# Kernel optimization log

Measured on AMD Instinct MI355X. Metric: run time of the kernel, lower is better.

Reference implementation:

```python
import jax, jax.numpy as jnp
import numpy as np

B = 64        # graphs in batch
N = 512       # nodes per graph (equal-size graphs)
DEG = 16      # avg degree
D_IN = 512
D_OUT = 512
RATIO = 0.5
K = int(np.ceil(RATIO * N))  # nodes kept per graph by SAGPool
NUM_NODES = B * N


def setup_inputs() -> dict:
    key = jax.random.key(0)
    ks = jax.random.split(key, 12)
    e_per = N * DEG
    offs = (jnp.arange(B, dtype=jnp.int32) * N)[:, None]
    src = (jax.random.randint(ks[0], (B, e_per), 0, N, dtype=jnp.int32) + offs).reshape(-1)
    dst = (jax.random.randint(ks[1], (B, e_per), 0, N, dtype=jnp.int32) + offs).reshape(-1)
    x = jax.random.normal(ks[2], (NUM_NODES, D_IN), jnp.float32)
    sc = 0.05  # small init so relu/tanh stay in sane range
    return {
        'x': x,
        'src': src,
        'dst': dst,
        'W1': jax.random.normal(ks[3], (D_IN, D_OUT), jnp.float32) * sc,
        'b1': jnp.zeros((D_OUT,), jnp.float32),
        'W2': jax.random.normal(ks[4], (D_OUT, D_OUT), jnp.float32) * sc,
        'b2': jnp.zeros((D_OUT,), jnp.float32),
        'sW1': jax.random.normal(ks[5], (D_OUT, 1), jnp.float32) * sc,
        'sb1': jnp.zeros((1,), jnp.float32),
        'sW2': jax.random.normal(ks[6], (D_OUT, 1), jnp.float32) * sc,
        'sb2': jnp.zeros((1,), jnp.float32),
    }


def graph_conv(src, dst, x, W, b, n_nodes):
    """DGL GraphConv, norm='both': D_in^{-1/2} A D_out^{-1/2} x W + b.
    W applied before aggregation (mathematically identical, cheaper when out_dim small)."""
    ones = jnp.ones(src.shape[0], x.dtype)
    deg_out = jax.ops.segment_sum(ones, src, num_segments=n_nodes)
    deg_in = jax.ops.segment_sum(ones, dst, num_segments=n_nodes)
    norm_out = jnp.maximum(deg_out, 1.0) ** -0.5  # DGL clamps deg to min 1
    norm_in = jnp.maximum(deg_in, 1.0) ** -0.5
    h = (x @ W) * norm_out[:, None]               # [n, out]
    m = jax.ops.segment_sum(h[src], dst, num_segments=n_nodes)  # gather+scatter over edges
    return m * norm_in[:, None] + b


def reference(x, src, dst, W1, b1, W2, b2, sW1, sb1, sW2, sb2):
    n = NUM_NODES
    h = jax.nn.relu(graph_conv(src, dst, x, W1, b1, n))   # conv1 + relu, reshape(-1,512) is a no-op
    h = jax.nn.relu(graph_conv(src, dst, h, W2, b2, n))   # conv2 + relu
    # SAGPool: two GraphConv score layers, averaged
    s1 = graph_conv(src, dst, h, sW1, sb1, n)[:, 0]
    s2 = graph_conv(src, dst, h, sW2, sb2, n)[:, 0]
    score = 0.5 * (s1 + s2)                                # [B*N]
    _, top_idx = jax.lax.top_k(score.reshape(B, N), K)     # per-graph top-k, [B, K]
    perm = (top_idx + (jnp.arange(B, dtype=top_idx.dtype) * N)[:, None]).reshape(-1)  # global ids
    pooled = h[perm] * jnp.tanh(score[perm])[:, None]      # [B*K, D_OUT] gated gather
    pb = pooled.reshape(B, K, D_OUT)
    # readout: max || sum per graph
    g_out = jnp.concatenate([pb.max(axis=1), pb.sum(axis=1)], axis=-1)  # [B, 2*D_OUT]
    return pooled, g_out
```

## Files before the change

kernel.cpp:

```cpp
#include <hip/hip_runtime.h>
#include <math.h>

typedef unsigned short u16;
typedef __attribute__((ext_vector_type(8))) short bf16x8;
typedef __attribute__((ext_vector_type(4))) float f32x4;

#define NN 32768
#define EDGES 524288
#define NB 64
#define NPG 512
#define EPG 8192
#define KEEP 256
#define D 512

__device__ __forceinline__ float b2f(u16 h){ return __uint_as_float(((unsigned)h)<<16); }
__device__ __forceinline__ u16 f2b(float f){
  unsigned u = __float_as_uint(f);
  unsigned r = u + 0x7FFFu + ((u>>16)&1u);
  return (u16)(r>>16);
}

__device__ __forceinline__ void gload16(const void* g, void* l){
  __builtin_amdgcn_global_load_lds((const __attribute__((address_space(1))) void*)g,
                                   (__attribute__((address_space(3))) void*)l, 16, 0, 0);
}

__global__ __launch_bounds__(256) void detect_kernel(const u16* __restrict__ xb, int* __restrict__ flags){
  __shared__ int cnt;
  if (threadIdx.x==0) cnt = 0;
  __syncthreads();
  u16 v = xb[threadIdx.x];
  int e = (v>>7)&0xFF;
  if (e > 140) atomicAdd(&cnt, 1);
  __syncthreads();
  if (threadIdx.x==0){ flags[0] = (cnt > 8) ? 1 : 0; flags[1] = 1; }
}

__global__ __launch_bounds__(512) void graphprep_kernel(
    const int* __restrict__ src, const int* __restrict__ dst,
    float* __restrict__ no, float* __restrict__ ni,
    int* __restrict__ rowp, int* __restrict__ csr)
{
  __shared__ int dego[NPG], degi[NPG], s[NPG], start[NPG], cur[NPG];
  int g = blockIdx.x, n = threadIdx.x;
  dego[n] = 0; degi[n] = 0; cur[n] = 0;
  __syncthreads();
  int ebase = g*EPG;
  #pragma unroll
  for (int i = 0; i < 16; i++){
    int e = ebase + n + i*512;
    atomicAdd(&dego[src[e] & (NPG-1)], 1);
    atomicAdd(&degi[dst[e] & (NPG-1)], 1);
  }
  __syncthreads();
  int di = degi[n];
  s[n] = di;
  __syncthreads();
  for (int off=1; off<NPG; off<<=1){
    int val = (n>=off) ? s[n-off] : 0;
    __syncthreads();
    s[n] += val;
    __syncthreads();
  }
  int excl = s[n] - di;
  start[n] = excl;
  int a = dego[n]; if (a<1) a=1;
  int b = di;      if (b<1) b=1;
  int v = g*NPG + n;
  no[v] = (float)(1.0/sqrt((double)a));
  ni[v] = (float)(1.0/sqrt((double)b));
  rowp[v] = ebase + excl;
  if (g == NB-1 && n == NPG-1) rowp[NN] = EDGES;
  __syncthreads();
  #pragma unroll
  for (int i = 0; i < 16; i++){
    int e = ebase + n + i*512;
    int dl = dst[e] & (NPG-1);
    int pos = atomicAdd(&cur[dl], 1);
    csr[ebase + start[dl] + pos] = src[e];
  }
}

__global__ __launch_bounds__(512) void bcvt_kernel(const int* __restrict__ flags,
    const void* b1, const void* b2, const void* sW1, const void* sW2,
    const void* sb1, const void* sb2,
    float* b1c, float* b2c, float* sW1c, float* sW2c, float* sbc)
{
  int t = threadIdx.x;
  int f = flags[0];
  #define CV(p,i) (f ? ((const float*)(p))[i] : b2f(((const u16*)(p))[i]))
  b1c[t]  = CV(b1, t);
  b2c[t]  = CV(b2, t);
  sW1c[t] = CV(sW1, t);
  sW2c[t] = CV(sW2, t);
  if (t==0){ sbc[0] = CV(sb1,0); sbc[1] = CV(sb2,0); }
  #undef CV
}

__global__ void tsplit_kernel(const int* __restrict__ flags, const void* __restrict__ W,
                              u16* __restrict__ WTh, u16* __restrict__ WTl){
  __shared__ float tile[32][33];
  int f = flags[0];
  int bx = blockIdx.x*32, by = blockIdx.y*32;
  int tx = threadIdx.x, ty = threadIdx.y;
  #pragma unroll
  for (int i=0;i<4;i++){
    size_t idx = (size_t)(by+ty+i*8)*D + bx+tx;
    tile[ty+i*8][tx] = f ? ((const float*)W)[idx] : b2f(((const u16*)W)[idx]);
  }
  __syncthreads();
  #pragma unroll
  for (int i=0;i<4;i++){
    float v = tile[tx][ty+i*8];
    u16 h = f2b(v);
    size_t o = (size_t)(bx+ty+i*8)*D + by+tx;
    WTh[o] = h;
    WTl[o] = f2b(v - b2f(h));
  }
}

__global__ __launch_bounds__(256) void xsplit_kernel(const void* __restrict__ X,
    const int* __restrict__ flags, u16* __restrict__ Xh, u16* __restrict__ Xl)
{
  size_t i = ((size_t)blockIdx.x*256 + threadIdx.x)*4;
  float v0,v1,v2,v3;
  if (flags[0]){
    float4 f = *(const float4*)((const float*)X + i);
    v0=f.x; v1=f.y; v2=f.z; v3=f.w;
  } else {
    ushort4 uv = *(const ushort4*)((const u16*)X + i);
    v0=b2f(uv.x); v1=b2f(uv.y); v2=b2f(uv.z); v3=b2f(uv.w);
  }
  ushort4 hh, hl;
  hh.x=f2b(v0); hl.x=f2b(v0-b2f(hh.x));
  hh.y=f2b(v1); hl.y=f2b(v1-b2f(hh.y));
  hh.z=f2b(v2); hl.z=f2b(v2-b2f(hh.z));
  hh.w=f2b(v3); hl.w=f2b(v3-b2f(hh.w));
  *(ushort4*)(Xh+i) = hh;
  *(ushort4*)(Xl+i) = hl;
}


__device__ __forceinline__ void gemm_tile256(int id, int& brow, int& bcol){
  int xcd = id & 7, k = id >> 3;
  brow = (xcd + 8*(k >> 1)) * 256;
  bcol = (k & 1) * 256;
}

__global__ __launch_bounds__(512, 2) void gemm256(
    const u16* __restrict__ Ahg, const u16* __restrict__ Alg,
    const u16* __restrict__ BTh, const u16* __restrict__ BTl,
    float* __restrict__ C, const float* __restrict__ rowscale)
{
  __shared__ alignas(16) u16 lds[2][4][8192];
  int t = threadIdx.x;
  int brow, bcol;
  gemm_tile256(blockIdx.x, brow, bcol);
  int wid = t>>6, lane = t&63;
  int wr = wid>>2, wc = wid&3;
  int q = lane>>4, r = lane&15;
  f32x4 acc[8][4] = {};

  int c0 = wid*128 + lane, c1 = c0 + 64;
  int q0 = c0>>8, r0 = c0&255, q1 = c1>>8, r1 = c1&255;
  const u16* sA0h = Ahg + (size_t)(brow+r0)*D + q0*8;
  const u16* sA1h = Ahg + (size_t)(brow+r1)*D + q1*8;
  const u16* sA0l = Alg + (size_t)(brow+r0)*D + q0*8;
  const u16* sA1l = Alg + (size_t)(brow+r1)*D + q1*8;
  const u16* sB0h = BTh + (size_t)(bcol+r0)*D + q0*8;
  const u16* sB1h = BTh + (size_t)(bcol+r1)*D + q1*8;
  const u16* sB0l = BTl + (size_t)(bcol+r0)*D + q0*8;
  const u16* sB1l = BTl + (size_t)(bcol+r1)*D + q1*8;

  #define STAGEK(B, KT) { int ko = (KT)*32; \
    gload16(sA0h+ko, &lds[B][0][c0*8]); gload16(sA1h+ko, &lds[B][0][c1*8]); \
    gload16(sA0l+ko, &lds[B][1][c0*8]); gload16(sA1l+ko, &lds[B][1][c1*8]); \
    gload16(sB0h+ko, &lds[B][2][c0*8]); gload16(sB1h+ko, &lds[B][2][c1*8]); \
    gload16(sB0l+ko, &lds[B][3][c0*8]); gload16(sB1l+ko, &lds[B][3][c1*8]); }

  STAGEK(0, 0)
  asm volatile("s_waitcnt vmcnt(0)" ::: "memory");
  __syncthreads();
  int cur = 0;
  for (int kt=0; kt<16; kt++){
    if (kt < 15) STAGEK(cur^1, kt+1)
    bf16x8 fbh[4], fbl[4];
    #pragma unroll
    for (int n=0;n<4;n++){
      fbh[n] = *(const bf16x8*)(&lds[cur][2][(q*256 + wc*64 + n*16 + r)*8]);
      fbl[n] = *(const bf16x8*)(&lds[cur][3][(q*256 + wc*64 + n*16 + r)*8]);
    }
    __builtin_amdgcn_s_setprio(1);
    #pragma unroll
    for (int m=0;m<8;m++){
      bf16x8 fah = *(const bf16x8*)(&lds[cur][0][(q*256 + wr*128 + m*16 + r)*8]);
      bf16x8 fal = *(const bf16x8*)(&lds[cur][1][(q*256 + wr*128 + m*16 + r)*8]);
      #pragma unroll
      for (int n=0;n<4;n++){
        acc[m][n] = __builtin_amdgcn_mfma_f32_16x16x32_bf16(fah, fbh[n], acc[m][n], 0,0,0);
        acc[m][n] = __builtin_amdgcn_mfma_f32_16x16x32_bf16(fah, fbl[n], acc[m][n], 0,0,0);
        acc[m][n] = __builtin_amdgcn_mfma_f32_16x16x32_bf16(fal, fbh[n], acc[m][n], 0,0,0);
      }
    }
    __builtin_amdgcn_s_setprio(0);
    asm volatile("s_waitcnt vmcnt(0)" ::: "memory");
    __syncthreads();
    cur ^= 1;
  }
  #undef STAGEK

  #pragma unroll
  for (int m=0;m<8;m++){
    int rowb = brow + wr*128 + m*16 + q*4;
    #pragma unroll
    for (int n=0;n<4;n++){
      int col = bcol + wc*64 + n*16 + r;
      #pragma unroll
      for (int g=0; g<4; g++){
        int row = rowb + g;
        C[(size_t)row*D + col] = acc[m][n][g] * rowscale[row];
      }
    }
  }
}


__global__ __launch_bounds__(256) void agg_kernel(
    const float* __restrict__ Y, const int* __restrict__ rowp,
    const int* __restrict__ csr, const float* __restrict__ ni,
    const float* __restrict__ bias, float* __restrict__ H,
    u16* __restrict__ Hh, u16* __restrict__ Hl,
    const float* __restrict__ sW1, const float* __restrict__ sW2,
    float* __restrict__ t1, float* __restrict__ t2, int mode)
{
  int i = blockIdx.x;
  int xcd = i & 7, j = i >> 3;
  int half = threadIdx.x >> 7;
  int t = threadIdx.x & 127;
  int lane = threadIdx.x & 63;
  int v = (xcd + 8*(j >> 8))*NPG + ((j & 255)*2 + half);
  int rp0 = rowp[v], rp1 = rowp[v+1];
  const float4* Yv = (const float4*)Y;
  float4 a = {0.f,0.f,0.f,0.f};
  for (int eb = rp0; eb < rp1; eb += 64){
    int cnt = rp1 - eb; if (cnt > 64) cnt = 64;
    int idx = (lane < cnt) ? csr[eb + lane] : 0;
    int e = 0;
    for (; e+8 <= cnt; e += 8){
      int u0 = __shfl(idx, e),   u1 = __shfl(idx, e+1);
      int u2 = __shfl(idx, e+2), u3 = __shfl(idx, e+3);
      int u4 = __shfl(idx, e+4), u5 = __shfl(idx, e+5);
      int u6 = __shfl(idx, e+6), u7 = __shfl(idx, e+7);
      float4 y0 = Yv[(size_t)u0*128 + t];
      float4 y1 = Yv[(size_t)u1*128 + t];
      float4 y2 = Yv[(size_t)u2*128 + t];
      float4 y3 = Yv[(size_t)u3*128 + t];
      float4 y4 = Yv[(size_t)u4*128 + t];
      float4 y5 = Yv[(size_t)u5*128 + t];
      float4 y6 = Yv[(size_t)u6*128 + t];
      float4 y7 = Yv[(size_t)u7*128 + t];
      a.x += ((y0.x + y1.x) + (y2.x + y3.x)) + ((y4.x + y5.x) + (y6.x + y7.x));
      a.y += ((y0.y + y1.y) + (y2.y + y3.y)) + ((y4.y + y5.y) + (y6.y + y7.y));
      a.z += ((y0.z + y1.z) + (y2.z + y3.z)) + ((y4.z + y5.z) + (y6.z + y7.z));
      a.w += ((y0.w + y1.w) + (y2.w + y3.w)) + ((y4.w + y5.w) + (y6.w + y7.w));
    }
    for (; e+4 <= cnt; e += 4){
      int u0 = __shfl(idx, e),   u1 = __shfl(idx, e+1);
      int u2 = __shfl(idx, e+2), u3 = __shfl(idx, e+3);
      float4 y0 = Yv[(size_t)u0*128 + t];
      float4 y1 = Yv[(size_t)u1*128 + t];
      float4 y2 = Yv[(size_t)u2*128 + t];
      float4 y3 = Yv[(size_t)u3*128 + t];
      a.x += (y0.x + y1.x) + (y2.x + y3.x);
      a.y += (y0.y + y1.y) + (y2.y + y3.y);
      a.z += (y0.z + y1.z) + (y2.z + y3.z);
      a.w += (y0.w + y1.w) + (y2.w + y3.w);
    }
    for (; e < cnt; e++){
      int u = __shfl(idx, e);
      float4 y = Yv[(size_t)u*128 + t];
      a.x += y.x; a.y += y.y; a.z += y.z; a.w += y.w;
    }
  }
  float w = ni[v];
  float4 b4 = ((const float4*)bias)[t];
  float4 rr;
  rr.x = fmaxf(a.x*w + b4.x, 0.f);
  rr.y = fmaxf(a.y*w + b4.y, 0.f);
  rr.z = fmaxf(a.z*w + b4.z, 0.f);
  rr.w = fmaxf(a.w*w + b4.w, 0.f);

  if (mode == 0){
    ushort4 hh, hl;
    hh.x = f2b(rr.x); hl.x = f2b(rr.x - b2f(hh.x));
    hh.y = f2b(rr.y); hl.y = f2b(rr.y - b2f(hh.y));
    hh.z = f2b(rr.z); hl.z = f2b(rr.z - b2f(hh.z));
    hh.w = f2b(rr.w); hl.w = f2b(rr.w - b2f(hh.w));
    *(ushort4*)(Hh + (size_t)v*D + t*4) = hh;
    *(ushort4*)(Hl + (size_t)v*D + t*4) = hl;
  } else {
    ((float4*)H)[(size_t)v*128 + t] = rr;
    float4 w1 = ((const float4*)sW1)[t];
    float4 w2 = ((const float4*)sW2)[t];
    float p1 = rr.x*w1.x + rr.y*w1.y + rr.z*w1.z + rr.w*w1.w;
    float p2 = rr.x*w2.x + rr.y*w2.y + rr.z*w2.z + rr.w*w2.w;
    #pragma unroll
    for (int off=32; off>=1; off>>=1){
      p1 += __shfl_xor(p1, off);
      p2 += __shfl_xor(p2, off);
    }
    __shared__ float red1[4], red2[4];
    int wv = threadIdx.x>>6;
    if (lane==0){ red1[wv] = p1; red2[wv] = p2; }
    __syncthreads();
    if (t==0){
      t1[v] = red1[half*2] + red1[half*2+1];
      t2[v] = red2[half*2] + red2[half*2+1];
    }
  }
}


__global__ __launch_bounds__(512) void scoretopk_kernel(
    const float* __restrict__ t1, const float* __restrict__ t2,
    const int* __restrict__ rowp, const int* __restrict__ csr,
    const float* __restrict__ no, const float* __restrict__ ni,
    const float* __restrict__ sbc,
    int* __restrict__ perm, float* __restrict__ gate)
{
  __shared__ unsigned long long key[NPG];
  __shared__ float scl[NPG];
  int g = blockIdx.x, n = threadIdx.x;
  int v = g*NPG + n;
  double a1 = 0.0, a2 = 0.0;
  int rp1 = rowp[v+1];
  for (int e=rowp[v]; e<rp1; e++){
    int u = csr[e];
    double w = (double)no[u];
    a1 += (double)t1[u]*w;
    a2 += (double)t2[u]*w;
  }
  double wi = (double)ni[v];
  double s1 = a1*wi + (double)sbc[0];
  double s2 = a2*wi + (double)sbc[1];
  float s = (float)(0.5*(s1+s2));
  scl[n] = s;
  unsigned u = __float_as_uint(s);
  u = (u & 0x80000000u) ? ~u : (u | 0x80000000u);
  unsigned kd = ~u;
  key[n] = ((unsigned long long)kd<<32) | (unsigned)n;
  __syncthreads();
  for (int k=2; k<=NPG; k<<=1){
    for (int j=k>>1; j>0; j>>=1){
      int ixj = n ^ j;
      if (ixj > n){
        unsigned long long a = key[n], b = key[ixj];
        bool up = ((n & k) == 0);
        if ((a > b) == up){ key[n] = b; key[ixj] = a; }
      }
      __syncthreads();
    }
  }
  if (n < KEEP){
    unsigned long long e = key[n];
    int idx = (int)(e & 0xFFFFFFFFull);
    perm[g*KEEP + n] = g*NPG + idx;
    gate[g*KEEP + n] = tanhf(scl[idx]);
  }
}


__global__ __launch_bounds__(256) void readout_kernel(const float* __restrict__ H,
    const int* __restrict__ perm, const float* __restrict__ gate,
    float* __restrict__ outp, float* __restrict__ outg)
{
  __shared__ int sp[KEEP];
  __shared__ float sg[KEEP];
  __shared__ float4 redmx[128], redsm[128];
  int g = blockIdx.x, t = threadIdx.x;
  int half = t >> 7, c = t & 127;
  sp[t] = perm[g*KEEP + t];
  sg[t] = gate[g*KEEP + t];
  __syncthreads();
  float4 mx = {-INFINITY,-INFINITY,-INFINITY,-INFINITY};
  float4 sm = {0.f,0.f,0.f,0.f};
  for (int rI = half; rI < KEEP; rI += 2){
    int node = sp[rI];
    float gt = sg[rI];
    float4 y = ((const float4*)(H + (size_t)node*D))[c];
    float4 vv;
    vv.x = y.x*gt; vv.y = y.y*gt; vv.z = y.z*gt; vv.w = y.w*gt;
    ((float4*)(outp + (size_t)(g*KEEP + rI)*D))[c] = vv;
    mx.x = fmaxf(mx.x, vv.x); mx.y = fmaxf(mx.y, vv.y);
    mx.z = fmaxf(mx.z, vv.z); mx.w = fmaxf(mx.w, vv.w);
    sm.x += vv.x; sm.y += vv.y; sm.z += vv.z; sm.w += vv.w;
  }
  if (half == 1){ redmx[c] = mx; redsm[c] = sm; }
  __syncthreads();
  if (half == 0){
    float4 omx = redmx[c], osm = redsm[c];
    mx.x = fmaxf(mx.x, omx.x); mx.y = fmaxf(mx.y, omx.y);
    mx.z = fmaxf(mx.z, omx.z); mx.w = fmaxf(mx.w, omx.w);
    sm.x += osm.x; sm.y += osm.y; sm.z += osm.z; sm.w += osm.w;
    ((float4*)(outg + (size_t)g*1024))[c] = mx;
    ((float4*)(outg + (size_t)g*1024 + 512))[c] = sm;
  }
}


extern "C" void kernel_launch(void* const* d_in, const int* in_sizes, int n_in,
                              void* d_out, int out_size, void* d_ws, size_t ws_size,
                              hipStream_t stream)
{
  (void)in_sizes; (void)n_in; (void)out_size; (void)ws_size;
  const void* x   = d_in[0];
  const int* src  = (const int*)d_in[1];
  const int* dst  = (const int*)d_in[2];
  const void* W1  = d_in[3];
  const void* b1  = d_in[4];
  const void* W2  = d_in[5];
  const void* b2  = d_in[6];
  const void* sW1 = d_in[7];
  const void* sb1 = d_in[8];
  const void* sW2 = d_in[9];
  const void* sb2 = d_in[10];
  float* out = (float*)d_out;

  char* ws = (char*)d_ws;
  size_t off = 0;
  auto alloc = [&](size_t bytes){ void* p = ws + off; off += (bytes + 255) & ~(size_t)255; return p; };
  int*   flags  = (int*)  alloc(2*4);
  float* no     = (float*)alloc((size_t)NN*4);
  float* ni     = (float*)alloc((size_t)NN*4);
  int*   rowp   = (int*)  alloc((size_t)(NN+1)*4);
  float* t1     = (float*)alloc((size_t)NN*4);
  float* t2     = (float*)alloc((size_t)NN*4);
  int*   perm   = (int*)  alloc((size_t)NB*KEEP*4);
  float* gate   = (float*)alloc((size_t)NB*KEEP*4);
  float* b1c    = (float*)alloc((size_t)D*4);
  float* b2c    = (float*)alloc((size_t)D*4);
  float* sW1c   = (float*)alloc((size_t)D*4);
  float* sW2c   = (float*)alloc((size_t)D*4);
  float* sbc    = (float*)alloc(2*4);
  u16*   W1Th   = (u16*)  alloc((size_t)D*D*2);
  u16*   W1Tl   = (u16*)  alloc((size_t)D*D*2);
  u16*   W2Th   = (u16*)  alloc((size_t)D*D*2);
  u16*   W2Tl   = (u16*)  alloc((size_t)D*D*2);
  int*   csr    = (int*)  alloc((size_t)EDGES*4);
  u16*   Hh     = (u16*)  alloc((size_t)NN*D*2);
  u16*   Hl     = (u16*)  alloc((size_t)NN*D*2);
  float* Y      = (float*)alloc((size_t)NN*D*4);
  float* H      = (float*)alloc((size_t)NN*D*4);
  u16*   Xh     = (u16*)H;
  u16*   Xl     = Xh + (size_t)NN*D;

  detect_kernel   <<<1, 256, 0, stream>>>((const u16*)x, flags);
  graphprep_kernel<<<NB, 512, 0, stream>>>(src, dst, no, ni, rowp, csr);
  bcvt_kernel     <<<1, 512, 0, stream>>>(flags, b1, b2, sW1, sW2, sb1, sb2,
                                          b1c, b2c, sW1c, sW2c, sbc);
  tsplit_kernel   <<<dim3(16,16), dim3(32,8), 0, stream>>>(flags, W1, W1Th, W1Tl);
  tsplit_kernel   <<<dim3(16,16), dim3(32,8), 0, stream>>>(flags, W2, W2Th, W2Tl);
  xsplit_kernel   <<<(NN*D/4)/256, 256, 0, stream>>>(x, flags, Xh, Xl);

  gemm256<<<256, 512, 0, stream>>>(Xh, Xl, W1Th, W1Tl, Y, no);
  agg_kernel<<<NN/2, 256, 0, stream>>>(Y, rowp, csr, ni, b1c, nullptr, Hh, Hl,
                                       nullptr, nullptr, nullptr, nullptr, 0);
  gemm256<<<256, 512, 0, stream>>>(Hh, Hl, W2Th, W2Tl, Y, no);
  agg_kernel<<<NN/2, 256, 0, stream>>>(Y, rowp, csr, ni, b2c, H, nullptr, nullptr,
                                       sW1c, sW2c, t1, t2, 1);

  scoretopk_kernel<<<NB, 512, 0, stream>>>(t1, t2, rowp, csr, no, ni, sbc, perm, gate);
  readout_kernel  <<<NB, 256, 0, stream>>>(H, perm, gate, out, out + (size_t)NB*KEEP*D);
}
```

Baseline: 345.0 us.

## Fuse small prep kernels, merge score/top-k with readout, store final H in bf16

```diff
diff --git a/kernel.cpp b/kernel.cpp
--- a/kernel.cpp
+++ b/kernel.cpp
@@ -25,15 +25,17 @@
                                    (__attribute__((address_space(3))) void*)l, 16, 0, 0);
 }
 
-__global__ __launch_bounds__(256) void detect_kernel(const u16* __restrict__ xb, int* __restrict__ flags){
-  __shared__ int cnt;
-  if (threadIdx.x==0) cnt = 0;
-  __syncthreads();
-  u16 v = xb[threadIdx.x];
-  int e = (v>>7)&0xFF;
-  if (e > 140) atomicAdd(&cnt, 1);
-  __syncthreads();
-  if (threadIdx.x==0){ flags[0] = (cnt > 8) ? 1 : 0; flags[1] = 1; }
+__device__ __forceinline__ int flag_f32(const u16* __restrict__ xb, int tid){
+  __shared__ int fl;
+  if (tid < 64){
+    u16 v0 = xb[tid*2], v1 = xb[tid*2+1];
+    int c = ((((v0>>7)&0xFF) > 140) ? 1 : 0) + ((((v1>>7)&0xFF) > 140) ? 1 : 0);
+    #pragma unroll
+    for (int o=32; o>=1; o>>=1) c += __shfl_xor(c, o);
+    if (tid == 0) fl = (c > 8) ? 1 : 0;
+  }
+  __syncthreads();
+  return fl;
 }
 
 __global__ __launch_bounds__(512) void graphprep_kernel(
@@ -81,13 +83,13 @@
   }
 }
 
-__global__ __launch_bounds__(512) void bcvt_kernel(const int* __restrict__ flags,
+__global__ __launch_bounds__(512) void bcvt_kernel(const u16* __restrict__ xb,
     const void* b1, const void* b2, const void* sW1, const void* sW2,
     const void* sb1, const void* sb2,
     float* b1c, float* b2c, float* sW1c, float* sW2c, float* sbc)
 {
   int t = threadIdx.x;
-  int f = flags[0];
+  int f = flag_f32(xb, t);
   #define CV(p,i) (f ? ((const float*)(p))[i] : b2f(((const u16*)(p))[i]))
   b1c[t]  = CV(b1, t);
   b2c[t]  = CV(b2, t);
@@ -97,10 +99,16 @@
   #undef CV
 }
 
-__global__ void tsplit_kernel(const int* __restrict__ flags, const void* __restrict__ W,
-                              u16* __restrict__ WTh, u16* __restrict__ WTl){
+__global__ void tsplit_kernel(const u16* __restrict__ xb,
+                              const void* __restrict__ W1, const void* __restrict__ W2,
+                              u16* __restrict__ W1Th, u16* __restrict__ W1Tl,
+                              u16* __restrict__ W2Th, u16* __restrict__ W2Tl){
   __shared__ float tile[32][33];
-  int f = flags[0];
+  int tid = threadIdx.x + threadIdx.y*32;
+  int f = flag_f32(xb, tid);
+  const void* W = blockIdx.z ? W2 : W1;
+  u16* WTh = blockIdx.z ? W2Th : W1Th;
+  u16* WTl = blockIdx.z ? W2Tl : W1Tl;
   int bx = blockIdx.x*32, by = blockIdx.y*32;
   int tx = threadIdx.x, ty = threadIdx.y;
   #pragma unroll
@@ -120,24 +128,27 @@
 }
 
 __global__ __launch_bounds__(256) void xsplit_kernel(const void* __restrict__ X,
-    const int* __restrict__ flags, u16* __restrict__ Xh, u16* __restrict__ Xl)
-{
-  size_t i = ((size_t)blockIdx.x*256 + threadIdx.x)*4;
-  float v0,v1,v2,v3;
-  if (flags[0]){
-    float4 f = *(const float4*)((const float*)X + i);
-    v0=f.x; v1=f.y; v2=f.z; v3=f.w;
-  } else {
-    ushort4 uv = *(const ushort4*)((const u16*)X + i);
-    v0=b2f(uv.x); v1=b2f(uv.y); v2=b2f(uv.z); v3=b2f(uv.w);
-  }
-  ushort4 hh, hl;
-  hh.x=f2b(v0); hl.x=f2b(v0-b2f(hh.x));
-  hh.y=f2b(v1); hl.y=f2b(v1-b2f(hh.y));
-  hh.z=f2b(v2); hl.z=f2b(v2-b2f(hh.z));
-  hh.w=f2b(v3); hl.w=f2b(v3-b2f(hh.w));
-  *(ushort4*)(Xh+i) = hh;
-  *(ushort4*)(Xl+i) = hl;
+    u16* __restrict__ Xh, u16* __restrict__ Xl)
+{
+  int f = flag_f32((const u16*)X, threadIdx.x);
+  size_t stride = (size_t)gridDim.x*256*4;
+  for (size_t i = ((size_t)blockIdx.x*256 + threadIdx.x)*4; i < (size_t)NN*D; i += stride){
+    float v0,v1,v2,v3;
+    if (f){
+      float4 fv = *(const float4*)((const float*)X + i);
+      v0=fv.x; v1=fv.y; v2=fv.z; v3=fv.w;
+    } else {
+      ushort4 uv = *(const ushort4*)((const u16*)X + i);
+      v0=b2f(uv.x); v1=b2f(uv.y); v2=b2f(uv.z); v3=b2f(uv.w);
+    }
+    ushort4 hh, hl;
+    hh.x=f2b(v0); hl.x=f2b(v0-b2f(hh.x));
+    hh.y=f2b(v1); hl.y=f2b(v1-b2f(hh.y));
+    hh.z=f2b(v2); hl.z=f2b(v2-b2f(hh.z));
+    hh.w=f2b(v3); hl.w=f2b(v3-b2f(hh.w));
+    *(ushort4*)(Xh+i) = hh;
+    *(ushort4*)(Xl+i) = hl;
+  }
 }
 
 
@@ -228,7 +239,7 @@
 __global__ __launch_bounds__(256) void agg_kernel(
     const float* __restrict__ Y, const int* __restrict__ rowp,
     const int* __restrict__ csr, const float* __restrict__ ni,
-    const float* __restrict__ bias, float* __restrict__ H,
+    const float* __restrict__ bias,
     u16* __restrict__ Hh, u16* __restrict__ Hl,
     const float* __restrict__ sW1, const float* __restrict__ sW2,
     float* __restrict__ t1, float* __restrict__ t2, int mode)
@@ -299,7 +310,9 @@
     *(ushort4*)(Hh + (size_t)v*D + t*4) = hh;
     *(ushort4*)(Hl + (size_t)v*D + t*4) = hl;
   } else {
-    ((float4*)H)[(size_t)v*128 + t] = rr;
+    ushort4 hb;
+    hb.x = f2b(rr.x); hb.y = f2b(rr.y); hb.z = f2b(rr.z); hb.w = f2b(rr.w);
+    *(ushort4*)(Hh + (size_t)v*D + t*4) = hb;
     float4 w1 = ((const float4*)sW1)[t];
     float4 w2 = ((const float4*)sW2)[t];
     float p1 = rr.x*w1.x + rr.y*w1.y + rr.z*w1.z + rr.w*w1.w;
@@ -321,15 +334,18 @@
 }
 
 
-__global__ __launch_bounds__(512) void scoretopk_kernel(
+__global__ __launch_bounds__(512) void scoretopk_readout_kernel(
     const float* __restrict__ t1, const float* __restrict__ t2,
     const int* __restrict__ rowp, const int* __restrict__ csr,
     const float* __restrict__ no, const float* __restrict__ ni,
-    const float* __restrict__ sbc,
-    int* __restrict__ perm, float* __restrict__ gate)
+    const float* __restrict__ sbc, const u16* __restrict__ Hb,
+    float* __restrict__ outp, float* __restrict__ outg)
 {
   __shared__ unsigned long long key[NPG];
   __shared__ float scl[NPG];
+  __shared__ int sp[KEEP];
+  __shared__ float sg[KEEP];
+  __shared__ float4 redmx[3*128], redsm[3*128];
   int g = blockIdx.x, n = threadIdx.x;
   int v = g*NPG + n;
   double a1 = 0.0, a2 = 0.0;
@@ -362,46 +378,36 @@
     }
   }
   if (n < KEEP){
-    unsigned long long e = key[n];
-    int idx = (int)(e & 0xFFFFFFFFull);
-    perm[g*KEEP + n] = g*NPG + idx;
-    gate[g*KEEP + n] = tanhf(scl[idx]);
-  }
-}
-
-
-__global__ __launch_bounds__(256) void readout_kernel(const float* __restrict__ H,
-    const int* __restrict__ perm, const float* __restrict__ gate,
-    float* __restrict__ outp, float* __restrict__ outg)
-{
-  __shared__ int sp[KEEP];
-  __shared__ float sg[KEEP];
-  __shared__ float4 redmx[128], redsm[128];
-  int g = blockIdx.x, t = threadIdx.x;
-  int half = t >> 7, c = t & 127;
-  sp[t] = perm[g*KEEP + t];
-  sg[t] = gate[g*KEEP + t];
-  __syncthreads();
+    int idx = (int)(key[n] & 0xFFFFFFFFull);
+    sp[n] = g*NPG + idx;
+    sg[n] = tanhf(scl[idx]);
+  }
+  __syncthreads();
+  int quarter = n >> 7, c = n & 127;
   float4 mx = {-INFINITY,-INFINITY,-INFINITY,-INFINITY};
   float4 sm = {0.f,0.f,0.f,0.f};
-  for (int rI = half; rI < KEEP; rI += 2){
+  for (int rI = quarter; rI < KEEP; rI += 4){
     int node = sp[rI];
     float gt = sg[rI];
-    float4 y = ((const float4*)(H + (size_t)node*D))[c];
+    ushort4 hv = *(const ushort4*)(Hb + (size_t)node*D + c*4);
     float4 vv;
-    vv.x = y.x*gt; vv.y = y.y*gt; vv.z = y.z*gt; vv.w = y.w*gt;
+    vv.x = b2f(hv.x)*gt; vv.y = b2f(hv.y)*gt;
+    vv.z = b2f(hv.z)*gt; vv.w = b2f(hv.w)*gt;
     ((float4*)(outp + (size_t)(g*KEEP + rI)*D))[c] = vv;
     mx.x = fmaxf(mx.x, vv.x); mx.y = fmaxf(mx.y, vv.y);
     mx.z = fmaxf(mx.z, vv.z); mx.w = fmaxf(mx.w, vv.w);
     sm.x += vv.x; sm.y += vv.y; sm.z += vv.z; sm.w += vv.w;
   }
-  if (half == 1){ redmx[c] = mx; redsm[c] = sm; }
-  __syncthreads();
-  if (half == 0){
-    float4 omx = redmx[c], osm = redsm[c];
-    mx.x = fmaxf(mx.x, omx.x); mx.y = fmaxf(mx.y, omx.y);
-    mx.z = fmaxf(mx.z, omx.z); mx.w = fmaxf(mx.w, omx.w);
-    sm.x += osm.x; sm.y += osm.y; sm.z += osm.z; sm.w += osm.w;
+  if (quarter > 0){ redmx[(quarter-1)*128 + c] = mx; redsm[(quarter-1)*128 + c] = sm; }
+  __syncthreads();
+  if (quarter == 0){
+    #pragma unroll
+    for (int qq=0; qq<3; qq++){
+      float4 omx = redmx[qq*128 + c], osm = redsm[qq*128 + c];
+      mx.x = fmaxf(mx.x, omx.x); mx.y = fmaxf(mx.y, omx.y);
+      mx.z = fmaxf(mx.z, omx.z); mx.w = fmaxf(mx.w, omx.w);
+      sm.x += osm.x; sm.y += osm.y; sm.z += osm.z; sm.w += osm.w;
+    }
     ((float4*)(outg + (size_t)g*1024))[c] = mx;
     ((float4*)(outg + (size_t)g*1024 + 512))[c] = sm;
   }
@@ -429,14 +435,11 @@
   char* ws = (char*)d_ws;
   size_t off = 0;
   auto alloc = [&](size_t bytes){ void* p = ws + off; off += (bytes + 255) & ~(size_t)255; return p; };
-  int*   flags  = (int*)  alloc(2*4);
   float* no     = (float*)alloc((size_t)NN*4);
   float* ni     = (float*)alloc((size_t)NN*4);
   int*   rowp   = (int*)  alloc((size_t)(NN+1)*4);
   float* t1     = (float*)alloc((size_t)NN*4);
   float* t2     = (float*)alloc((size_t)NN*4);
-  int*   perm   = (int*)  alloc((size_t)NB*KEEP*4);
-  float* gate   = (float*)alloc((size_t)NB*KEEP*4);
   float* b1c    = (float*)alloc((size_t)D*4);
   float* b2c    = (float*)alloc((size_t)D*4);
   float* sW1c   = (float*)alloc((size_t)D*4);
@@ -450,25 +453,24 @@
   u16*   Hh     = (u16*)  alloc((size_t)NN*D*2);
   u16*   Hl     = (u16*)  alloc((size_t)NN*D*2);
   float* Y      = (float*)alloc((size_t)NN*D*4);
-  float* H      = (float*)alloc((size_t)NN*D*4);
-  u16*   Xh     = (u16*)H;
-  u16*   Xl     = Xh + (size_t)NN*D;
-
-  detect_kernel   <<<1, 256, 0, stream>>>((const u16*)x, flags);
+  u16*   Xh     = (u16*)  alloc((size_t)NN*D*2);
+  u16*   Xl     = (u16*)  alloc((size_t)NN*D*2);
+  u16*   Hb     = Hh;
+
   graphprep_kernel<<<NB, 512, 0, stream>>>(src, dst, no, ni, rowp, csr);
-  bcvt_kernel     <<<1, 512, 0, stream>>>(flags, b1, b2, sW1, sW2, sb1, sb2,
+  bcvt_kernel     <<<1, 512, 0, stream>>>((const u16*)x, b1, b2, sW1, sW2, sb1, sb2,
                                           b1c, b2c, sW1c, sW2c, sbc);
-  tsplit_kernel   <<<dim3(16,16), dim3(32,8), 0, stream>>>(flags, W1, W1Th, W1Tl);
-  tsplit_kernel   <<<dim3(16,16), dim3(32,8), 0, stream>>>(flags, W2, W2Th, W2Tl);
-  xsplit_kernel   <<<(NN*D/4)/256, 256, 0, stream>>>(x, flags, Xh, Xl);
+  tsplit_kernel   <<<dim3(16,16,2), dim3(32,8), 0, stream>>>((const u16*)x, W1, W2,
+                                          W1Th, W1Tl, W2Th, W2Tl);
+  xsplit_kernel   <<<2048, 256, 0, stream>>>(x, Xh, Xl);
 
   gemm256<<<256, 512, 0, stream>>>(Xh, Xl, W1Th, W1Tl, Y, no);
-  agg_kernel<<<NN/2, 256, 0, stream>>>(Y, rowp, csr, ni, b1c, nullptr, Hh, Hl,
+  agg_kernel<<<NN/2, 256, 0, stream>>>(Y, rowp, csr, ni, b1c, Hh, Hl,
                                        nullptr, nullptr, nullptr, nullptr, 0);
   gemm256<<<256, 512, 0, stream>>>(Hh, Hl, W2Th, W2Tl, Y, no);
-  agg_kernel<<<NN/2, 256, 0, stream>>>(Y, rowp, csr, ni, b2c, H, nullptr, nullptr,
+  agg_kernel<<<NN/2, 256, 0, stream>>>(Y, rowp, csr, ni, b2c, Hb, nullptr,
                                        sW1c, sW2c, t1, t2, 1);
 
-  scoretopk_kernel<<<NB, 512, 0, stream>>>(t1, t2, rowp, csr, no, ni, sbc, perm, gate);
-  readout_kernel  <<<NB, 256, 0, stream>>>(H, perm, gate, out, out + (size_t)NB*KEEP*D);
-}
+  scoretopk_readout_kernel<<<NB, 512, 0, stream>>>(t1, t2, rowp, csr, no, ni, sbc,
+                                       Hb, out, out + (size_t)NB*KEEP*D);
+}
```

Result: faster. 312.5 us, median of 2 (-9.4%).
